# Optimization experiments

Measured on AMD Instinct MI355X. Metric: run time of the kernel, lower is better.

## Reference

```python
import jax, jax.numpy as jnp
import numpy as np

B, P, D, H, L = 1024, 22, 3, 64, 4
HS = P + 1  # 22-dim one-hot atom type + 1 time channel
N = B * P


def _edges():
    # fully-connected directed edges (no self loops) per graph, batched with node offsets
    idx = np.arange(P)
    r, c = np.meshgrid(idx, idx, indexing='ij')
    m = r != c
    r0, c0 = r[m], c[m]
    off = (P * np.arange(B))[:, None]
    row = (r0[None, :] + off).reshape(-1)
    col = (c0[None, :] + off).reshape(-1)
    return row.astype(np.int32), col.astype(np.int32)


def setup_inputs() -> dict:
    key = jax.random.key(0)
    ks = jax.random.split(key, 12)
    s = 0.02
    row, col = _edges()
    return dict(
        input_array=jax.random.normal(ks[0], (B, P * D), jnp.float32),
        time_array=jax.random.uniform(ks[1], (B,), jnp.float32),
        emb_w=jax.random.normal(ks[2], (HS, H), jnp.float32) * s,
        emb_b=jnp.zeros((H,), jnp.float32),
        edge_w1=jax.random.normal(ks[3], (L, 2 * H + 2, H), jnp.float32) * s,
        edge_b1=jnp.zeros((L, H), jnp.float32),
        edge_w2=jax.random.normal(ks[4], (L, H, H), jnp.float32) * s,
        edge_b2=jnp.zeros((L, H), jnp.float32),
        node_w1=jax.random.normal(ks[5], (L, 2 * H, H), jnp.float32) * s,
        node_b1=jnp.zeros((L, H), jnp.float32),
        node_w2=jax.random.normal(ks[6], (L, H, H), jnp.float32) * s,
        node_b2=jnp.zeros((L, H), jnp.float32),
        cm_w1=jax.random.normal(ks[7], (L, H, H), jnp.float32) * s,
        cm_b1=jnp.zeros((L, H), jnp.float32),
        cm_w2=jax.random.normal(ks[8], (L, H, 1), jnp.float32) * 0.001,  # xavier gain=0.001 final layer
        cc_w1=jax.random.normal(ks[9], (L, H, H), jnp.float32) * s,
        cc_b1=jnp.zeros((L, H), jnp.float32),
        cc_w2=jax.random.normal(ks[10], (L, H, 1), jnp.float32) * 0.001,
        row=jnp.asarray(row),
        col=jnp.asarray(col),
    )


def reference(input_array, time_array, emb_w, emb_b, edge_w1, edge_b1, edge_w2, edge_b2,
              node_w1, node_b1, node_w2, node_b2, cm_w1, cm_b1, cm_w2,
              cc_w1, cc_b1, cc_w2, row, col):
    silu = jax.nn.silu
    x0 = input_array.reshape(N, D)
    # h_initial: one-hot atom types repeated over batch, plus time channel
    h = jnp.tile(jnp.eye(P, dtype=input_array.dtype), (B, 1))  # [N, 22]
    t = jnp.repeat(time_array[:, None], P, axis=1).reshape(N, 1)
    h = jnp.concatenate([h, t], axis=1)  # [N, 23]
    # edge_attr = squared distance at initial coords (fixed across layers)
    edge_attr = jnp.sum((x0[row] - x0[col]) ** 2, axis=1, keepdims=True)  # [E,1]
    h = h @ emb_w + emb_b  # embedding
    x = x0
    seg = lambda d: jax.ops.segment_sum(d, row, num_segments=N)
    for l in range(L):
        diff = x[row] - x[col]                                   # [E,3]
        radial = jnp.sum(diff ** 2, axis=1, keepdims=True)       # [E,1]
        coord_diff = diff / (jnp.sqrt(radial + 1e-8) + 1)
        e_in = jnp.concatenate([h[row], h[col], radial, edge_attr], axis=1)
        ef = silu(silu(e_in @ edge_w1[l] + edge_b1[l]) @ edge_w2[l] + edge_b2[l])  # [E,H]
        cross = jnp.cross(x[row], x[col])                        # [E,3]
        cross = cross / (jnp.sqrt(jnp.sum(cross ** 2, axis=1, keepdims=True) + 1e-8) + 1)
        cm = silu(ef @ cm_w1[l] + cm_b1[l]) @ cm_w2[l]           # [E,1]
        cc = silu(ef @ cc_w1[l] + cc_b1[l]) @ cc_w2[l]           # [E,1]
        trans = coord_diff * cm + cc * cross                     # [E,3]
        x = x + seg(trans)                                       # agg='sum'
        agg = jnp.concatenate([h, seg(ef)], axis=1)              # [N,2H]
        h = h + (silu(agg @ node_w1[l] + node_b1[l]) @ node_w2[l] + node_b2[l])  # recurrent
    vel = (x - x0).reshape(B, P, D)
    vel = vel - jnp.mean(vel, axis=1, keepdims=True)  # remove_mean
    return vel.reshape(B, P * D)
```

## Files before the change

### kernel.cpp

```cpp
#include <hip/hip_runtime.h>
#include <hip/hip_bf16.h>
#include <math.h>

#define PP 22
#define HH 64
#define NL 4
#define NE 462
#define NTILE 29
#define SST 68

typedef __attribute__((ext_vector_type(8))) short bf16x8;
typedef __attribute__((ext_vector_type(4))) float f32x4;

#define MFMA(A, B, C) __builtin_amdgcn_mfma_f32_16x16x32_bf16(A, B, C, 0, 0, 0)
#define PHI(mt, r) ((((mt) >> 1) << 5) + (((r) >> 2) << 3) + (((mt) & 1) << 2) + ((r) & 3))

__device__ __forceinline__ float silu_f(float v) { return v / (1.0f + __expf(-v)); }

__device__ __forceinline__ unsigned short f2bf(float x) {
    __hip_bfloat16 h = __float2bfloat16(x);
    unsigned short u;
    __builtin_memcpy(&u, &h, 2);
    return u;
}

#define LD8(dst, PTR) { \
    float4 _a = *(const float4*)(PTR); float4 _b = *(const float4*)((PTR) + 4); \
    dst[0]=_a.x; dst[1]=_a.y; dst[2]=_a.z; dst[3]=_a.w; \
    dst[4]=_b.x; dst[5]=_b.y; dst[6]=_b.z; dst[7]=_b.w; }

__global__ __launch_bounds__(64) void prep_w(
    const float* __restrict__ edge_w1, const float* __restrict__ edge_w2,
    const float* __restrict__ cm_w1, const float* __restrict__ cc_w1,
    const float* __restrict__ node_w1, const float* __restrict__ node_w2,
    unsigned short* __restrict__ ws)
{
    int blk = blockIdx.x;
    int l = blk >> 6, moff = blk & 63;
    int lane = threadIdx.x, n0 = lane & 15, kg = lane >> 4;
    const float* base; int col, kt;
    if (moff < 8)       { kt = moff >> 2;              int nt = moff & 3;        base = edge_w1 + l * 130 * HH;           col = nt * 16 + n0; }
    else if (moff < 16) { int m = moff - 8;  kt = m >> 2; int nt = m & 3;        base = edge_w1 + l * 130 * HH + 64 * HH; col = nt * 16 + n0; }
    else if (moff < 24) { int m = moff - 16; kt = m >> 2; int mt = m & 3;        base = edge_w2 + l * HH * HH;            col = PHI(mt, n0); }
    else if (moff < 32) { int m = moff - 24; kt = m >> 2; int nt = m & 3;        base = cm_w1 + l * HH * HH;              col = nt * 16 + n0; }
    else if (moff < 40) { int m = moff - 32; kt = m >> 2; int nt = m & 3;        base = cc_w1 + l * HH * HH;              col = nt * 16 + n0; }
    else if (moff < 56) { int m = moff - 40; kt = m >> 2; int mt = m & 3;        base = node_w1 + l * 128 * HH;           col = PHI(mt, n0); }
    else                { int m = moff - 56; kt = m >> 2; int nt = m & 3;        base = node_w2 + l * HH * HH;            col = nt * 16 + n0; }
    int k0 = kt * 32 + kg * 8;
    unsigned short* d = ws + blk * 512 + lane * 8;
#pragma unroll
    for (int j = 0; j < 8; ++j) d[j] = f2bf(base[(k0 + j) * HH + col]);
}

__global__ __launch_bounds__(256, 4) void egnn_kernel(
    const float* __restrict__ input, const float* __restrict__ timev,
    const float* __restrict__ emb_w, const float* __restrict__ emb_b,
    const float* __restrict__ edge_w1, const float* __restrict__ edge_b1,
    const float* __restrict__ edge_b2,
    const float* __restrict__ node_b1, const float* __restrict__ node_b2,
    const float* __restrict__ cm_b1, const float* __restrict__ cm_w2,
    const float* __restrict__ cc_b1, const float* __restrict__ cc_w2,
    const unsigned short* __restrict__ wfr,
    float* __restrict__ out)
{
    const int g    = blockIdx.x;
    const int tid  = threadIdx.x;
    const int w    = tid >> 6;
    const int lane = tid & 63;
    const int n0   = lane & 15;
    const int kg   = lane >> 4;

    __shared__ float sApre[PP][SST], sBpre[PP][SST];
    __shared__ float sh[PP][SST], sSeg[PP][SST];
    __shared__ float scd[NE][3], scr[NE][3];
    __shared__ __align__(16) float sx[PP][4];
    __shared__ __align__(16) float sx0[PP][4];
    __shared__ float sTr[PP][4];
    __shared__ float sW128[HH], sW129[HH];
    __shared__ float sBp[128];
    __shared__ float sHC[256];
    __shared__ float smean[3];

    if (tid < PP * 3) {
        float v = input[g * (PP * 3) + tid];
        sx0[tid / 3][tid % 3] = v;
        sx [tid / 3][tid % 3] = v;
    }
    if (tid < PP) { sx0[tid][3] = 0.f; sx[tid][3] = 0.f; }
    {
        float tg = timev[g];
        for (int i = w; i < PP; i += 4)
            sh[i][lane] = emb_w[i * HH + lane] + tg * emb_w[PP * HH + lane] + emb_b[lane];
    }
    for (int idx = tid; idx < PP * SST; idx += 256) (&sSeg[0][0])[idx] = 0.f;
    if (tid < PP * 4) (&sTr[0][0])[tid] = 0.f;
    __syncthreads();

    for (int l = 0; l < NL; ++l) {
        const unsigned short* wfl = wfr + (size_t)l * 32768;

        for (int e = tid; e < NE; e += 256) {
            int a = e % PP, r = e / PP;
            int b = (r < a) ? r : r + 1;
            float4 xa = *(const float4*)&sx[a][0];
            float4 xb = *(const float4*)&sx[b][0];
            float dx = xa.x - xb.x, dy = xa.y - xb.y, dz = xa.z - xb.z;
            float rad = dx * dx + dy * dy + dz * dz;
            float inv = 1.0f / (sqrtf(rad + 1e-8f) + 1.0f);
            scd[e][0] = dx * inv; scd[e][1] = dy * inv; scd[e][2] = dz * inv;
            float cx = xa.y * xb.z - xa.z * xb.y;
            float cy = xa.z * xb.x - xa.x * xb.z;
            float cz = xa.x * xb.y - xa.y * xb.x;
            float cn = 1.0f / (sqrtf(cx * cx + cy * cy + cz * cz + 1e-8f) + 1.0f);
            scr[e][0] = cx * cn; scr[e][1] = cy * cn; scr[e][2] = cz * cn;
        }
        if (tid < HH)          sW128[tid]      = edge_w1[(l * 130 + 128) * HH + tid];
        else if (tid < 2 * HH) sW129[tid - HH] = edge_w1[(l * 130 + 129) * HH + tid - HH];
        if (tid < 128) {
            int i = tid & 63, mt = i >> 4, r = i & 15;
            int phi = PHI(mt, r);
            sBp[tid] = (tid < 64) ? edge_b2[l * HH + phi] : node_b1[l * HH + phi];
        }
        {
            int i = tid & 63, arr = tid >> 6;
            const float* src = (arr == 0) ? cm_b1 : (arr == 1) ? cc_b1 : (arr == 2) ? cm_w2 : cc_w2;
            sHC[tid] = src[l * HH + i];
        }
        {
            int mtn = w & 1, mat = w >> 1;
            int node = mtn * 16 + n0;
            bool vn = node < PP;
            int crow = vn ? node : 0;
            bf16x8 hhi[2];
#pragma unroll
            for (int kt = 0; kt < 2; ++kt) {
                float vv[8];
                LD8(vv, &sh[crow][kt * 32 + kg * 8]);
#pragma unroll
                for (int j = 0; j < 8; ++j)
                    hhi[kt][j] = (short)f2bf(vn ? vv[j] : 0.f);
            }
#pragma unroll
            for (int ntf = 0; ntf < 4; ++ntf) {
                f32x4 acc = (f32x4){0.f, 0.f, 0.f, 0.f};
#pragma unroll
                for (int kt = 0; kt < 2; ++kt) {
                    bf16x8 wv = *(const bf16x8*)(wfl + (mat * 8 + kt * 4 + ntf) * 512 + lane * 8);
                    acc = MFMA(hhi[kt], wv, acc);
                }
                int col = ntf * 16 + n0;
                float b1v = edge_b1[l * HH + col];
#pragma unroll
                for (int q = 0; q < 4; ++q) {
                    int m = mtn * 16 + kg * 4 + q;
                    if (m < PP) {
                        if (mat == 0) sApre[m][col] = acc[q] + b1v;
                        else          sBpre[m][col] = acc[q];
                    }
                }
            }
        }
        __syncthreads();

        for (int jt = w; jt < NTILE; jt += 4) {
            int e0 = jt * 16;
            int e = e0 + n0;
            bool vr = e < NE;
            int ec = vr ? e : (NE - 1);
            int a = ec % PP, r = ec / PP;
            int b = (r < a) ? r : r + 1;
            float4 xa = *(const float4*)&sx[a][0];
            float4 xb = *(const float4*)&sx[b][0];
            float4 oa = *(const float4*)&sx0[a][0];
            float4 ob = *(const float4*)&sx0[b][0];
            float dx = xa.x - xb.x, dy = xa.y - xb.y, dz = xa.z - xb.z;
            float rad = dx * dx + dy * dy + dz * dz;
            float ex = oa.x - ob.x, ey = oa.y - ob.y, ez = oa.z - ob.z;
            float ea = ex * ex + ey * ey + ez * ez;

            f32x4 acc[4];
#pragma unroll
            for (int mt = 0; mt < 4; ++mt) acc[mt] = (f32x4){0.f, 0.f, 0.f, 0.f};
#pragma unroll
            for (int kt = 0; kt < 2; ++kt) {
                int base = kt * 32 + kg * 8;
                float av[8], bv[8], w8[8], w9[8];
                LD8(av, &sApre[a][base]);
                LD8(bv, &sBpre[b][base]);
                LD8(w8, &sW128[base]);
                LD8(w9, &sW129[base]);
                bf16x8 zhi;
#pragma unroll
                for (int j8 = 0; j8 < 8; ++j8) {
                    float z = av[j8] + bv[j8] + rad * w8[j8] + ea * w9[j8];
                    zhi[j8] = (short)f2bf(silu_f(z));
                }
#pragma unroll
                for (int mt = 0; mt < 4; ++mt) {
                    bf16x8 wv = *(const bf16x8*)(wfl + (16 + kt * 4 + mt) * 512 + lane * 8);
                    acc[mt] = MFMA(wv, zhi, acc[mt]);
                }
            }
            unsigned short pk[4][4];
#pragma unroll
            for (int mt = 0; mt < 4; ++mt) {
                int phib = ((mt >> 1) << 5) + (kg << 3) + ((mt & 1) << 2);
#pragma unroll
                for (int q = 0; q < 4; ++q) {
                    float v = silu_f(acc[mt][q] + sBp[mt * 16 + kg * 4 + q]);
                    v = vr ? v : 0.f;
                    pk[mt][q] = f2bf(v);
                    if (vr) atomicAdd(&sSeg[a][phib + q], v);
                }
            }
            bf16x8 ehi[2];
#pragma unroll
            for (int kt = 0; kt < 2; ++kt)
#pragma unroll
                for (int j8 = 0; j8 < 8; ++j8)
                    ehi[kt][j8] = (short)pk[kt * 2 + (j8 >> 2)][j8 & 3];

            float pm[4] = {0.f, 0.f, 0.f, 0.f}, pc[4] = {0.f, 0.f, 0.f, 0.f};
#pragma unroll
            for (int nt = 0; nt < 4; ++nt) {
                f32x4 am = (f32x4){0.f, 0.f, 0.f, 0.f};
                f32x4 ac = (f32x4){0.f, 0.f, 0.f, 0.f};
#pragma unroll
                for (int kt = 0; kt < 2; ++kt) {
                    bf16x8 cmw = *(const bf16x8*)(wfl + (24 + kt * 4 + nt) * 512 + lane * 8);
                    bf16x8 ccw = *(const bf16x8*)(wfl + (32 + kt * 4 + nt) * 512 + lane * 8);
                    am = MFMA(ehi[kt], cmw, am);
                    ac = MFMA(ehi[kt], ccw, ac);
                }
                float cmb = sHC[nt * 16 + n0];
                float ccb = sHC[64 + nt * 16 + n0];
                float cm2 = sHC[128 + nt * 16 + n0];
                float cc2 = sHC[192 + nt * 16 + n0];
#pragma unroll
                for (int q = 0; q < 4; ++q) {
                    pm[q] += silu_f(am[q] + cmb) * cm2;
                    pc[q] += silu_f(ac[q] + ccb) * cc2;
                }
            }
#pragma unroll
            for (int q = 0; q < 4; ++q) {
#pragma unroll
                for (int off = 1; off <= 8; off <<= 1) {
                    pm[q] += __shfl_xor(pm[q], off);
                    pc[q] += __shfl_xor(pc[q], off);
                }
            }
            if (n0 < 3) {
#pragma unroll
                for (int q = 0; q < 4; ++q) {
                    int gE = e0 + kg * 4 + q;
                    if (gE < NE) {
                        int a2 = gE % PP;
                        atomicAdd(&sTr[a2][n0], scd[gE][n0] * pm[q] + pc[q] * scr[gE][n0]);
                    }
                }
            }
        }
        __syncthreads();

        unsigned short pk[4][4];
        {
            int mtn = w >> 1;
            int node = mtn * 16 + n0;
            bool vn = node < PP;
            int crow = vn ? node : 0;
            f32x4 acc[4];
#pragma unroll
            for (int mt = 0; mt < 4; ++mt) acc[mt] = (f32x4){0.f, 0.f, 0.f, 0.f};
#pragma unroll
            for (int kt = 0; kt < 4; ++kt) {
                const float* srcp = (kt < 2) ? &sh[crow][kt * 32 + kg * 8]
                                             : &sSeg[crow][(kt - 2) * 32 + kg * 8];
                float vv[8];
                LD8(vv, srcp);
                bf16x8 bhi;
#pragma unroll
                for (int j8 = 0; j8 < 8; ++j8)
                    bhi[j8] = (short)f2bf(vn ? vv[j8] : 0.f);
#pragma unroll
                for (int mt = 0; mt < 4; ++mt) {
                    bf16x8 wv = *(const bf16x8*)(wfl + (40 + kt * 4 + mt) * 512 + lane * 8);
                    acc[mt] = MFMA(wv, bhi, acc[mt]);
                }
            }
#pragma unroll
            for (int mt = 0; mt < 4; ++mt)
#pragma unroll
                for (int q = 0; q < 4; ++q)
                    pk[mt][q] = f2bf(silu_f(acc[mt][q] + sBp[64 + mt * 16 + kg * 4 + q]));
        }
        __syncthreads();

        {
            bf16x8 mh[2];
#pragma unroll
            for (int kt = 0; kt < 2; ++kt)
#pragma unroll
                for (int j8 = 0; j8 < 8; ++j8)
                    mh[kt][j8] = (short)pk[kt * 2 + (j8 >> 2)][j8 & 3];
            int mtn = w >> 1;
#pragma unroll
            for (int t = 0; t < 2; ++t) {
                int ntf = (w & 1) * 2 + t;
                f32x4 acc = (f32x4){0.f, 0.f, 0.f, 0.f};
#pragma unroll
                for (int kt = 0; kt < 2; ++kt) {
                    bf16x8 wv = *(const bf16x8*)(wfl + (56 + kt * 4 + ntf) * 512 + lane * 8);
                    acc = MFMA(mh[kt], wv, acc);
                }
                int col = ntf * 16 + n0;
                float nb2 = node_b2[l * HH + col];
#pragma unroll
                for (int q = 0; q < 4; ++q) {
                    int m = mtn * 16 + kg * 4 + q;
                    if (m < PP) sh[m][col] += acc[q] + nb2;
                }
            }
        }
        if (tid < PP * 4) {
            int p = tid >> 2, d = tid & 3;
            float v = sTr[p][d];
            if (d < 3) sx[p][d] += v;
            sTr[p][d] = 0.f;
        }
        for (int idx = tid; idx < PP * SST; idx += 256) (&sSeg[0][0])[idx] = 0.f;
        __syncthreads();
    }

    if (tid < 3) {
        float s = 0.0f;
        for (int p = 0; p < PP; ++p) s += sx[p][tid] - sx0[p][tid];
        smean[tid] = s / (float)PP;
    }
    __syncthreads();
    if (tid < PP * 3) {
        int p = tid / 3, d = tid % 3;
        out[g * (PP * 3) + tid] = (sx[p][d] - sx0[p][d]) - smean[d];
    }
}

extern "C" void kernel_launch(void* const* d_in, const int* in_sizes, int n_in,
                              void* d_out, int out_size, void* d_ws, size_t ws_size,
                              hipStream_t stream) {
    const float* input   = (const float*)d_in[0];
    const float* timev   = (const float*)d_in[1];
    const float* emb_w   = (const float*)d_in[2];
    const float* emb_b   = (const float*)d_in[3];
    const float* edge_w1 = (const float*)d_in[4];
    const float* edge_b1 = (const float*)d_in[5];
    const float* edge_w2 = (const float*)d_in[6];
    const float* edge_b2 = (const float*)d_in[7];
    const float* node_w1 = (const float*)d_in[8];
    const float* node_b1 = (const float*)d_in[9];
    const float* node_w2 = (const float*)d_in[10];
    const float* node_b2 = (const float*)d_in[11];
    const float* cm_w1   = (const float*)d_in[12];
    const float* cm_b1   = (const float*)d_in[13];
    const float* cm_w2   = (const float*)d_in[14];
    const float* cc_w1   = (const float*)d_in[15];
    const float* cc_b1   = (const float*)d_in[16];
    const float* cc_w2   = (const float*)d_in[17];

    unsigned short* wsu = (unsigned short*)d_ws;
    prep_w<<<dim3(NL * 64), dim3(64), 0, stream>>>(edge_w1, edge_w2, cm_w1, cc_w1,
                                                   node_w1, node_w2, wsu);

    float* out = (float*)d_out;
    egnn_kernel<<<dim3(1024), dim3(256), 0, stream>>>(
        input, timev, emb_w, emb_b, edge_w1, edge_b1, edge_b2,
        node_b1, node_b2, cm_b1, cm_w2, cc_b1, cc_w2, wsu, out);
}
```

Before: 881.4 us.

## Process two graphs per block and stage bf16 weight fragments in LDS

Each block now handles two graphs with 512 threads, and the per-layer bf16 weight fragments are copied into a shared LDS buffer in three phases instead of being read from global memory by every wave. The precomputed coord_diff/cross arrays are removed; each edge lane recomputes them in registers, and the per-edge cm/cc scalars are broadcast through a small LDS scratch so three atomics per edge replace the per-dimension scatter. This is meant to amortise weight loads across two graphs and cut global traffic and LDS footprint. In exchange it adds extra __syncthreads for staging, fewer blocks overall (512 instead of 1024), and possible occupancy loss from the larger LDS use.

```diff
diff --git a/kernel.cpp b/kernel.cpp
--- a/kernel.cpp
+++ b/kernel.cpp
@@ -14,6 +14,7 @@
 
 #define MFMA(A, B, C) __builtin_amdgcn_mfma_f32_16x16x32_bf16(A, B, C, 0, 0, 0)
 #define PHI(mt, r) ((((mt) >> 1) << 5) + (((r) >> 2) << 3) + (((mt) & 1) << 2) + ((r) & 3))
+#define WAVE_SYNC() asm volatile("s_waitcnt lgkmcnt(0)" ::: "memory")
 
 __device__ __forceinline__ float silu_f(float v) { return v / (1.0f + __expf(-v)); }
 
@@ -52,7 +53,7 @@
     for (int j = 0; j < 8; ++j) d[j] = f2bf(base[(k0 + j) * HH + col]);
 }
 
-__global__ __launch_bounds__(256, 4) void egnn_kernel(
+__global__ __launch_bounds__(512, 2) void egnn_kernel(
     const float* __restrict__ input, const float* __restrict__ timev,
     const float* __restrict__ emb_w, const float* __restrict__ emb_b,
     const float* __restrict__ edge_w1, const float* __restrict__ edge_b1,
@@ -63,71 +64,67 @@
     const unsigned short* __restrict__ wfr,
     float* __restrict__ out)
 {
-    const int g    = blockIdx.x;
+    const int g0   = blockIdx.x * 2;
     const int tid  = threadIdx.x;
     const int w    = tid >> 6;
+    const int lw   = w & 3;
+    const int gi   = w >> 2;
     const int lane = tid & 63;
     const int n0   = lane & 15;
     const int kg   = lane >> 4;
 
-    __shared__ float sApre[PP][SST], sBpre[PP][SST];
-    __shared__ float sh[PP][SST], sSeg[PP][SST];
-    __shared__ float scd[NE][3], scr[NE][3];
-    __shared__ __align__(16) float sx[PP][4];
-    __shared__ __align__(16) float sx0[PP][4];
-    __shared__ float sTr[PP][4];
+    __shared__ __align__(16) unsigned short wlds[12288];
+    __shared__ float sApre[2][PP][SST], sBpre[2][PP][SST];
+    __shared__ float sh[2][PP][SST], sSeg[2][PP][SST];
+    __shared__ __align__(16) float sx[2][PP][4];
+    __shared__ __align__(16) float sx0[2][PP][4];
+    __shared__ float sTr[2][PP][4];
     __shared__ float sW128[HH], sW129[HH];
     __shared__ float sBp[128];
     __shared__ float sHC[256];
-    __shared__ float smean[3];
-
-    if (tid < PP * 3) {
-        float v = input[g * (PP * 3) + tid];
-        sx0[tid / 3][tid % 3] = v;
-        sx [tid / 3][tid % 3] = v;
-    }
-    if (tid < PP) { sx0[tid][3] = 0.f; sx[tid][3] = 0.f; }
+    __shared__ float swPm[8][16], swPc[8][16];
+    __shared__ float smean[2][3];
+
+#define STAGE(SRC, N16) { const uint4* _s = (const uint4*)(SRC); uint4* _d = (uint4*)wlds; \
+    for (int idx = tid; idx < (N16); idx += 512) _d[idx] = _s[idx]; }
+
+    if (tid < 2 * PP * 3) {
+        int gg = tid / (PP * 3), j = tid % (PP * 3);
+        float v = input[(g0 + gg) * (PP * 3) + j];
+        sx0[gg][j / 3][j % 3] = v;
+        sx [gg][j / 3][j % 3] = v;
+    }
+    if (tid < 2 * PP) { int gg = tid / PP, p = tid % PP; sx0[gg][p][3] = 0.f; sx[gg][p][3] = 0.f; }
     {
-        float tg = timev[g];
-        for (int i = w; i < PP; i += 4)
-            sh[i][lane] = emb_w[i * HH + lane] + tg * emb_w[PP * HH + lane] + emb_b[lane];
-    }
-    for (int idx = tid; idx < PP * SST; idx += 256) (&sSeg[0][0])[idx] = 0.f;
-    if (tid < PP * 4) (&sTr[0][0])[tid] = 0.f;
+        float tg = timev[g0 + gi];
+        for (int i = lw; i < PP; i += 4)
+            sh[gi][i][lane] = emb_w[i * HH + lane] + tg * emb_w[PP * HH + lane] + emb_b[lane];
+    }
+    for (int idx = tid; idx < 2 * PP * SST; idx += 512) (&sSeg[0][0][0])[idx] = 0.f;
+    if (tid < 2 * PP * 4) (&sTr[0][0][0])[tid] = 0.f;
     __syncthreads();
 
     for (int l = 0; l < NL; ++l) {
         const unsigned short* wfl = wfr + (size_t)l * 32768;
 
-        for (int e = tid; e < NE; e += 256) {
-            int a = e % PP, r = e / PP;
-            int b = (r < a) ? r : r + 1;
-            float4 xa = *(const float4*)&sx[a][0];
-            float4 xb = *(const float4*)&sx[b][0];
-            float dx = xa.x - xb.x, dy = xa.y - xb.y, dz = xa.z - xb.z;
-            float rad = dx * dx + dy * dy + dz * dz;
-            float inv = 1.0f / (sqrtf(rad + 1e-8f) + 1.0f);
-            scd[e][0] = dx * inv; scd[e][1] = dy * inv; scd[e][2] = dz * inv;
-            float cx = xa.y * xb.z - xa.z * xb.y;
-            float cy = xa.z * xb.x - xa.x * xb.z;
-            float cz = xa.x * xb.y - xa.y * xb.x;
-            float cn = 1.0f / (sqrtf(cx * cx + cy * cy + cz * cz + 1e-8f) + 1.0f);
-            scr[e][0] = cx * cn; scr[e][1] = cy * cn; scr[e][2] = cz * cn;
-        }
-        if (tid < HH)          sW128[tid]      = edge_w1[(l * 130 + 128) * HH + tid];
-        else if (tid < 2 * HH) sW129[tid - HH] = edge_w1[(l * 130 + 129) * HH + tid - HH];
-        if (tid < 128) {
-            int i = tid & 63, mt = i >> 4, r = i & 15;
+        STAGE(wfl, 1024);
+        if (tid < HH)               sW128[tid]        = edge_w1[(l * 130 + 128) * HH + tid];
+        else if (tid < 2 * HH)      sW129[tid - HH]   = edge_w1[(l * 130 + 129) * HH + tid - HH];
+        else if (tid < 2 * HH + 128) {
+            int t2 = tid - 2 * HH;
+            int i = t2 & 63, mt = i >> 4, r = i & 15;
             int phi = PHI(mt, r);
-            sBp[tid] = (tid < 64) ? edge_b2[l * HH + phi] : node_b1[l * HH + phi];
-        }
+            sBp[t2] = (t2 < 64) ? edge_b2[l * HH + phi] : node_b1[l * HH + phi];
+        } else if (tid < 2 * HH + 128 + 256) {
+            int t3 = tid - (2 * HH + 128);
+            int i = t3 & 63, arr = t3 >> 6;
+            const float* src = (arr == 0) ? cm_b1 : (arr == 1) ? cc_b1 : (arr == 2) ? cm_w2 : cc_w2;
+            sHC[t3] = src[l * HH + i];
+        }
+        __syncthreads();
+
         {
-            int i = tid & 63, arr = tid >> 6;
-            const float* src = (arr == 0) ? cm_b1 : (arr == 1) ? cc_b1 : (arr == 2) ? cm_w2 : cc_w2;
-            sHC[tid] = src[l * HH + i];
-        }
-        {
-            int mtn = w & 1, mat = w >> 1;
+            int mtn = lw & 1, mat = lw >> 1;
             int node = mtn * 16 + n0;
             bool vn = node < PP;
             int crow = vn ? node : 0;
@@ -135,7 +132,7 @@
 #pragma unroll
             for (int kt = 0; kt < 2; ++kt) {
                 float vv[8];
-                LD8(vv, &sh[crow][kt * 32 + kg * 8]);
+                LD8(vv, &sh[gi][crow][kt * 32 + kg * 8]);
 #pragma unroll
                 for (int j = 0; j < 8; ++j)
                     hhi[kt][j] = (short)f2bf(vn ? vv[j] : 0.f);
@@ -145,7 +142,7 @@
                 f32x4 acc = (f32x4){0.f, 0.f, 0.f, 0.f};
 #pragma unroll
                 for (int kt = 0; kt < 2; ++kt) {
-                    bf16x8 wv = *(const bf16x8*)(wfl + (mat * 8 + kt * 4 + ntf) * 512 + lane * 8);
+                    bf16x8 wv = *(const bf16x8*)&wlds[(mat * 8 + kt * 4 + ntf) * 512 + lane * 8];
                     acc = MFMA(hhi[kt], wv, acc);
                 }
                 int col = ntf * 16 + n0;
@@ -154,29 +151,39 @@
                 for (int q = 0; q < 4; ++q) {
                     int m = mtn * 16 + kg * 4 + q;
                     if (m < PP) {
-                        if (mat == 0) sApre[m][col] = acc[q] + b1v;
-                        else          sBpre[m][col] = acc[q];
+                        if (mat == 0) sApre[gi][m][col] = acc[q] + b1v;
+                        else          sBpre[gi][m][col] = acc[q];
                     }
                 }
             }
         }
         __syncthreads();
 
-        for (int jt = w; jt < NTILE; jt += 4) {
+        STAGE(wfl + 16 * 512, 1536);
+        __syncthreads();
+
+        for (int jt = lw; jt < NTILE; jt += 4) {
             int e0 = jt * 16;
             int e = e0 + n0;
             bool vr = e < NE;
             int ec = vr ? e : (NE - 1);
             int a = ec % PP, r = ec / PP;
             int b = (r < a) ? r : r + 1;
-            float4 xa = *(const float4*)&sx[a][0];
-            float4 xb = *(const float4*)&sx[b][0];
-            float4 oa = *(const float4*)&sx0[a][0];
-            float4 ob = *(const float4*)&sx0[b][0];
+            float4 xa = *(const float4*)&sx[gi][a][0];
+            float4 xb = *(const float4*)&sx[gi][b][0];
+            float4 oa = *(const float4*)&sx0[gi][a][0];
+            float4 ob = *(const float4*)&sx0[gi][b][0];
             float dx = xa.x - xb.x, dy = xa.y - xb.y, dz = xa.z - xb.z;
             float rad = dx * dx + dy * dy + dz * dz;
             float ex = oa.x - ob.x, ey = oa.y - ob.y, ez = oa.z - ob.z;
             float ea = ex * ex + ey * ey + ez * ez;
+            float inv = 1.0f / (sqrtf(rad + 1e-8f) + 1.0f);
+            float cdx = dx * inv, cdy = dy * inv, cdz = dz * inv;
+            float cx = xa.y * xb.z - xa.z * xb.y;
+            float cy = xa.z * xb.x - xa.x * xb.z;
+            float cz = xa.x * xb.y - xa.y * xb.x;
+            float cn = 1.0f / (sqrtf(cx * cx + cy * cy + cz * cz + 1e-8f) + 1.0f);
+            float crx = cx * cn, cry = cy * cn, crz = cz * cn;
 
             f32x4 acc[4];
 #pragma unroll
@@ -185,8 +192,8 @@
             for (int kt = 0; kt < 2; ++kt) {
                 int base = kt * 32 + kg * 8;
                 float av[8], bv[8], w8[8], w9[8];
-                LD8(av, &sApre[a][base]);
-                LD8(bv, &sBpre[b][base]);
+                LD8(av, &sApre[gi][a][base]);
+                LD8(bv, &sBpre[gi][b][base]);
                 LD8(w8, &sW128[base]);
                 LD8(w9, &sW129[base]);
                 bf16x8 zhi;
@@ -197,11 +204,11 @@
                 }
 #pragma unroll
                 for (int mt = 0; mt < 4; ++mt) {
-                    bf16x8 wv = *(const bf16x8*)(wfl + (16 + kt * 4 + mt) * 512 + lane * 8);
+                    bf16x8 wv = *(const bf16x8*)&wlds[(kt * 4 + mt) * 512 + lane * 8];
                     acc[mt] = MFMA(wv, zhi, acc[mt]);
                 }
             }
-            unsigned short pk[4][4];
+            unsigned short pkE[4][4];
 #pragma unroll
             for (int mt = 0; mt < 4; ++mt) {
                 int phib = ((mt >> 1) << 5) + (kg << 3) + ((mt & 1) << 2);
@@ -209,8 +216,8 @@
                 for (int q = 0; q < 4; ++q) {
                     float v = silu_f(acc[mt][q] + sBp[mt * 16 + kg * 4 + q]);
                     v = vr ? v : 0.f;
-                    pk[mt][q] = f2bf(v);
-                    if (vr) atomicAdd(&sSeg[a][phib + q], v);
+                    pkE[mt][q] = f2bf(v);
+                    if (vr) atomicAdd(&sSeg[gi][a][phib + q], v);
                 }
             }
             bf16x8 ehi[2];
@@ -218,7 +225,7 @@
             for (int kt = 0; kt < 2; ++kt)
 #pragma unroll
                 for (int j8 = 0; j8 < 8; ++j8)
-                    ehi[kt][j8] = (short)pk[kt * 2 + (j8 >> 2)][j8 & 3];
+                    ehi[kt][j8] = (short)pkE[kt * 2 + (j8 >> 2)][j8 & 3];
 
             float pm[4] = {0.f, 0.f, 0.f, 0.f}, pc[4] = {0.f, 0.f, 0.f, 0.f};
 #pragma unroll
@@ -227,8 +234,8 @@
                 f32x4 ac = (f32x4){0.f, 0.f, 0.f, 0.f};
 #pragma unroll
                 for (int kt = 0; kt < 2; ++kt) {
-                    bf16x8 cmw = *(const bf16x8*)(wfl + (24 + kt * 4 + nt) * 512 + lane * 8);
-                    bf16x8 ccw = *(const bf16x8*)(wfl + (32 + kt * 4 + nt) * 512 + lane * 8);
+                    bf16x8 cmw = *(const bf16x8*)&wlds[(8 + kt * 4 + nt) * 512 + lane * 8];
+                    bf16x8 ccw = *(const bf16x8*)&wlds[(16 + kt * 4 + nt) * 512 + lane * 8];
                     am = MFMA(ehi[kt], cmw, am);
                     ac = MFMA(ehi[kt], ccw, ac);
                 }
@@ -250,22 +257,31 @@
                     pc[q] += __shfl_xor(pc[q], off);
                 }
             }
-            if (n0 < 3) {
-#pragma unroll
-                for (int q = 0; q < 4; ++q) {
-                    int gE = e0 + kg * 4 + q;
-                    if (gE < NE) {
-                        int a2 = gE % PP;
-                        atomicAdd(&sTr[a2][n0], scd[gE][n0] * pm[q] + pc[q] * scr[gE][n0]);
-                    }
-                }
-            }
-        }
-        __syncthreads();
-
-        unsigned short pk[4][4];
+            if (n0 == 0) {
+#pragma unroll
+                for (int q = 0; q < 4; ++q) {
+                    swPm[w][kg * 4 + q] = pm[q];
+                    swPc[w][kg * 4 + q] = pc[q];
+                }
+            }
+            WAVE_SYNC();
+            float pmv = swPm[w][n0];
+            float pcv = swPc[w][n0];
+            if (kg == 0 && vr) {
+                atomicAdd(&sTr[gi][a][0], cdx * pmv + pcv * crx);
+                atomicAdd(&sTr[gi][a][1], cdy * pmv + pcv * cry);
+                atomicAdd(&sTr[gi][a][2], cdz * pmv + pcv * crz);
+            }
+            WAVE_SYNC();
+        }
+        __syncthreads();
+
+        STAGE(wfl + 40 * 512, 1536);
+        __syncthreads();
+
+        unsigned short pkN[4][4];
         {
-            int mtn = w >> 1;
+            int mtn = lw >> 1;
             int node = mtn * 16 + n0;
             bool vn = node < PP;
             int crow = vn ? node : 0;
@@ -274,8 +290,8 @@
             for (int mt = 0; mt < 4; ++mt) acc[mt] = (f32x4){0.f, 0.f, 0.f, 0.f};
 #pragma unroll
             for (int kt = 0; kt < 4; ++kt) {
-                const float* srcp = (kt < 2) ? &sh[crow][kt * 32 + kg * 8]
-                                             : &sSeg[crow][(kt - 2) * 32 + kg * 8];
+                const float* srcp = (kt < 2) ? &sh[gi][crow][kt * 32 + kg * 8]
+                                             : &sSeg[gi][crow][(kt - 2) * 32 + kg * 8];
                 float vv[8];
                 LD8(vv, srcp);
                 bf16x8 bhi;
@@ -284,7 +300,7 @@
                     bhi[j8] = (short)f2bf(vn ? vv[j8] : 0.f);
 #pragma unroll
                 for (int mt = 0; mt < 4; ++mt) {
-                    bf16x8 wv = *(const bf16x8*)(wfl + (40 + kt * 4 + mt) * 512 + lane * 8);
+                    bf16x8 wv = *(const bf16x8*)&wlds[(kt * 4 + mt) * 512 + lane * 8];
                     acc[mt] = MFMA(wv, bhi, acc[mt]);
                 }
             }
@@ -292,7 +308,7 @@
             for (int mt = 0; mt < 4; ++mt)
 #pragma unroll
                 for (int q = 0; q < 4; ++q)
-                    pk[mt][q] = f2bf(silu_f(acc[mt][q] + sBp[64 + mt * 16 + kg * 4 + q]));
+                    pkN[mt][q] = f2bf(silu_f(acc[mt][q] + sBp[64 + mt * 16 + kg * 4 + q]));
         }
         __syncthreads();
 
@@ -302,15 +318,15 @@
             for (int kt = 0; kt < 2; ++kt)
 #pragma unroll
                 for (int j8 = 0; j8 < 8; ++j8)
-                    mh[kt][j8] = (short)pk[kt * 2 + (j8 >> 2)][j8 & 3];
-            int mtn = w >> 1;
+                    mh[kt][j8] = (short)pkN[kt * 2 + (j8 >> 2)][j8 & 3];
+            int mtn = lw >> 1;
 #pragma unroll
             for (int t = 0; t < 2; ++t) {
-                int ntf = (w & 1) * 2 + t;
+                int ntf = (lw & 1) * 2 + t;
                 f32x4 acc = (f32x4){0.f, 0.f, 0.f, 0.f};
 #pragma unroll
                 for (int kt = 0; kt < 2; ++kt) {
-                    bf16x8 wv = *(const bf16x8*)(wfl + (56 + kt * 4 + ntf) * 512 + lane * 8);
+                    bf16x8 wv = *(const bf16x8*)&wlds[(16 + kt * 4 + ntf) * 512 + lane * 8];
                     acc = MFMA(mh[kt], wv, acc);
                 }
                 int col = ntf * 16 + n0;
@@ -318,30 +334,34 @@
 #pragma unroll
                 for (int q = 0; q < 4; ++q) {
                     int m = mtn * 16 + kg * 4 + q;
-                    if (m < PP) sh[m][col] += acc[q] + nb2;
-                }
-            }
-        }
-        if (tid < PP * 4) {
-            int p = tid >> 2, d = tid & 3;
-            float v = sTr[p][d];
-            if (d < 3) sx[p][d] += v;
-            sTr[p][d] = 0.f;
-        }
-        for (int idx = tid; idx < PP * SST; idx += 256) (&sSeg[0][0])[idx] = 0.f;
-        __syncthreads();
-    }
-
-    if (tid < 3) {
+                    if (m < PP) sh[gi][m][col] += acc[q] + nb2;
+                }
+            }
+        }
+        if (tid < 2 * PP * 4) {
+            int gg = tid / (PP * 4), j = tid % (PP * 4);
+            int p = j >> 2, d = j & 3;
+            float v = sTr[gg][p][d];
+            if (d < 3) sx[gg][p][d] += v;
+            sTr[gg][p][d] = 0.f;
+        }
+        for (int idx = tid; idx < 2 * PP * SST; idx += 512) (&sSeg[0][0][0])[idx] = 0.f;
+        __syncthreads();
+    }
+
+    if (tid < 6) {
+        int gg = tid / 3, d = tid % 3;
         float s = 0.0f;
-        for (int p = 0; p < PP; ++p) s += sx[p][tid] - sx0[p][tid];
-        smean[tid] = s / (float)PP;
+        for (int p = 0; p < PP; ++p) s += sx[gg][p][d] - sx0[gg][p][d];
+        smean[gg][d] = s / (float)PP;
     }
     __syncthreads();
-    if (tid < PP * 3) {
-        int p = tid / 3, d = tid % 3;
-        out[g * (PP * 3) + tid] = (sx[p][d] - sx0[p][d]) - smean[d];
-    }
+    if (tid < 2 * PP * 3) {
+        int gg = tid / (PP * 3), j = tid % (PP * 3);
+        int p = j / 3, d = j % 3;
+        out[(g0 + gg) * (PP * 3) + j] = (sx[gg][p][d] - sx0[gg][p][d]) - smean[gg][d];
+    }
+#undef STAGE
 }
 
 extern "C" void kernel_launch(void* const* d_in, const int* in_sizes, int n_in,
@@ -371,7 +391,7 @@
                                                    node_w1, node_w2, wsu);
 
     float* out = (float*)d_out;
-    egnn_kernel<<<dim3(1024), dim3(256), 0, stream>>>(
+    egnn_kernel<<<dim3(512), dim3(512), 0, stream>>>(
         input, timev, emb_w, emb_b, edge_w1, edge_b1, edge_b2,
         node_b1, node_b2, cm_b1, cm_w2, cc_b1, cc_w2, wsu, out);
 }
```

Result: no change. 877.4 us (-0.5%).
